# Kernel optimization log

Hardware: AMD Instinct MI355X
Metric: run time of the kernel (lower is better)

The kernel has to match this reference:

```python
import jax, jax.numpy as jnp
import numpy as np

N, E, D_IN, HID, HEADS, D_OUT, R = 20000, 640000, 256, 128, 4, 128, 32
NEG_SLOPE = 0.2  # PyG GATConv default


def setup_inputs() -> dict:
    key = jax.random.key(0)
    ks = jax.random.split(key, 12)
    s = 0.05
    return {
        "x": jax.random.normal(ks[0], (N, D_IN), jnp.float32),
        "edge_index": jax.random.randint(ks[1], (2, E), 0, N, dtype=jnp.int64),
        "edge_type": jax.random.randint(ks[2], (E,), 0, R, dtype=jnp.int64),
        "rel_emb": jax.random.normal(ks[3], (R, D_IN), jnp.float32) * s,
        "W1": jax.random.normal(ks[4], (D_IN, HEADS * HID), jnp.float32) * s,
        "att_src1": jax.random.normal(ks[5], (HEADS, HID), jnp.float32) * s,
        "att_dst1": jax.random.normal(ks[6], (HEADS, HID), jnp.float32) * s,
        "b1": jnp.zeros((HEADS * HID,), jnp.float32),
        "W2": jax.random.normal(ks[7], (HEADS * HID, D_OUT), jnp.float32) * s,
        "att_src2": jax.random.normal(ks[8], (1, D_OUT), jnp.float32) * s,
        "att_dst2": jax.random.normal(ks[9], (1, D_OUT), jnp.float32) * s,
        "b2": jnp.zeros((D_OUT,), jnp.float32),
    }


def _gat_conv(x, src, dst, W, a_src, a_dst, bias, heads, ch):
    """PyG GATConv (eval mode, self loops already in src/dst)."""
    n = x.shape[0]
    h = (x @ W).reshape(n, heads, ch)                      # [N,H,C]
    alpha_s = jnp.einsum('nhc,hc->nh', h, a_src)           # [N,H]
    alpha_d = jnp.einsum('nhc,hc->nh', h, a_dst)
    e = jax.nn.leaky_relu(alpha_s[src] + alpha_d[dst], NEG_SLOPE)  # [E,H]
    # segment softmax over incoming edges of each dst node
    m = jax.ops.segment_max(e, dst, num_segments=n)        # [N,H]
    p = jnp.exp(e - m[dst])
    denom = jax.ops.segment_sum(p, dst, num_segments=n)
    alpha = p / (denom[dst] + 1e-16)                       # [E,H]
    out = jax.ops.segment_sum(h[src] * alpha[:, :, None], dst, num_segments=n)
    return out.reshape(n, heads * ch) + bias


def reference(x, edge_index, edge_type, rel_emb, W1, att_src1, att_dst1, b1,
              W2, att_src2, att_dst2, b2):
    src, dst = edge_index[0], edge_index[1]
    # relational feature injection: x_mod[src] += rel_emb[edge_type]
    x_mod = x.at[src].add(rel_emb[edge_type])
    # GATConv adds self loops by default
    loop = jnp.arange(N, dtype=src.dtype)
    s2 = jnp.concatenate([src, loop])
    d2 = jnp.concatenate([dst, loop])
    h = _gat_conv(x_mod, s2, d2, W1, att_src1, att_dst1, b1, HEADS, HID)
    h = jax.nn.elu(h)
    return _gat_conv(h, s2, d2, W2, att_src2, att_dst2, b2, 1, D_OUT)
```

## Files before the change

kernel.cpp:

```cpp
#include <hip/hip_runtime.h>


#define D_IN   256
#define HID1   512
#define NHEADS 4
#define DOUT   128
#define NREL   32
#define NEG_SLOPE 0.2f
#define M_PAD  20096
#define NB     128

static __device__ __forceinline__ unsigned short f2b(float f) {
  union { float f; unsigned int i; } v; v.f = f;
  unsigned int x = v.i;
  return (unsigned short)((x + 0x7fffu + ((x >> 16) & 1u)) >> 16);
}
static __device__ __forceinline__ float lrelu(float x) {
  return x > 0.f ? x : NEG_SLOPE * x;
}

typedef __attribute__((ext_vector_type(8))) short bf16x8;
typedef __attribute__((ext_vector_type(4))) float f32x4;
typedef __attribute__((ext_vector_type(2))) float f32x2;

static __device__ __forceinline__ f32x2 up2(unsigned int u) {
  union { unsigned int i; float f; } lo, hi;
  lo.i = u << 16; hi.i = u & 0xffff0000u;
  f32x2 v; v.x = lo.f; v.y = hi.f; return v;
}
static __device__ __forceinline__ void pkfma(f32x2& a, f32x2 b, f32x2 c) {
  asm("v_pk_fma_f32 %0, %1, %2, %0" : "+v"(a) : "v"(b), "v"(c));
}
static __device__ __forceinline__ void accp(f32x2* acc, float w, uint4 r) {
  f32x2 wv = (f32x2)(w);
  pkfma(acc[0], wv, up2(r.x));
  pkfma(acc[1], wv, up2(r.y));
  pkfma(acc[2], wv, up2(r.z));
  pkfma(acc[3], wv, up2(r.w));
}
static __device__ __forceinline__ void acc4(f32x2 acc[4][4], float* den,
                                            float4 av, float4 adv, uint4 r) {
  float w0 = __expf(lrelu(av.x + adv.x));
  float w1 = __expf(lrelu(av.y + adv.y));
  float w2 = __expf(lrelu(av.z + adv.z));
  float w3 = __expf(lrelu(av.w + adv.w));
  f32x2 x0 = up2(r.x), x1 = up2(r.y), x2 = up2(r.z), x3 = up2(r.w);
  f32x2 wv;
  wv = (f32x2)(w0);
  pkfma(acc[0][0], wv, x0); pkfma(acc[0][1], wv, x1);
  pkfma(acc[0][2], wv, x2); pkfma(acc[0][3], wv, x3);
  wv = (f32x2)(w1);
  pkfma(acc[1][0], wv, x0); pkfma(acc[1][1], wv, x1);
  pkfma(acc[1][2], wv, x2); pkfma(acc[1][3], wv, x3);
  wv = (f32x2)(w2);
  pkfma(acc[2][0], wv, x0); pkfma(acc[2][1], wv, x1);
  pkfma(acc[2][2], wv, x2); pkfma(acc[2][3], wv, x3);
  wv = (f32x2)(w3);
  pkfma(acc[3][0], wv, x0); pkfma(acc[3][1], wv, x1);
  pkfma(acc[3][2], wv, x2); pkfma(acc[3][3], wv, x3);
  den[0] += w0; den[1] += w1; den[2] += w2; den[3] += w3;
}

__global__ __launch_bounds__(256) void hist_prep_kernel(
    const int* __restrict__ src, const int* __restrict__ dst,
    const int* __restrict__ et, unsigned int* __restrict__ counts8,
    int* __restrict__ gtable, int E, int n, int cb,
    const float* __restrict__ W1, const float* __restrict__ W2,
    unsigned short* __restrict__ W1T, unsigned short* __restrict__ W2T,
    const float* __restrict__ att_s1, const float* __restrict__ att_d1,
    float* __restrict__ us4, float* __restrict__ ud4,
    const float* __restrict__ att_s2, const float* __restrict__ att_d2,
    float* __restrict__ vs, float* __restrict__ vd) {
  int b = blockIdx.x;
  int t = threadIdx.x;
  if (b < NB) {
    extern __shared__ int hist[];
    for (int i = t; i < n; i += 256) hist[i] = 0;
    __syncthreads();
    int per = (E + NB - 1) / NB;
    int e0 = b * per;
    int e1 = min(e0 + per, E);
    for (int e = e0 + t; e < e1; e += 256) {
      atomicAdd(&hist[dst[e]], 1);
      int s = src[e], r = et[e];
      atomicAdd(&counts8[(size_t)s * 8 + (r >> 2)], 1u << (8 * (r & 3)));
    }
    __syncthreads();
    for (int i = t; i < n; i += 256) gtable[(size_t)b * n + i] = hist[i];
  } else if (b < NB + cb) {
    int idx = (b - NB) * 256 + t;
    if (idx < D_IN * HID1) {
      int r = idx / HID1, c = idx % HID1;
      W1T[(size_t)c * D_IN + r] = f2b(W1[idx]);
    } else {
      int k = idx - D_IN * HID1;
      if (k < HID1 * DOUT) {
        int r = k / DOUT, c = k % DOUT;
        W2T[(size_t)c * HID1 + r] = f2b(W2[k]);
      }
    }
  } else if (b == NB + cb) {
    int k = t;
    float us[4] = {0.f, 0.f, 0.f, 0.f}, ud[4] = {0.f, 0.f, 0.f, 0.f};
    for (int h = 0; h < 4; ++h)
      for (int c = 0; c < 128; ++c) {
        float wv = W1[(size_t)k * HID1 + h * 128 + c];
        us[h] += wv * att_s1[h * 128 + c];
        ud[h] += wv * att_d1[h * 128 + c];
      }
    ((float4*)us4)[k] = make_float4(us[0], us[1], us[2], us[3]);
    ((float4*)ud4)[k] = make_float4(ud[0], ud[1], ud[2], ud[3]);
  } else {
#pragma unroll
    for (int rr = 0; rr < 2; ++rr) {
      int r = t * 2 + rr;
      float ss = 0.f, dd = 0.f;
      for (int c = 0; c < DOUT; ++c) {
        float wv = W2[(size_t)r * DOUT + c];
        ss += wv * att_s2[c];
        dd += wv * att_d2[c];
      }
      vs[r] = ss; vd[r] = dd;
    }
  }
}

__global__ void colsum_kernel(const int* __restrict__ gtable,
                              int* __restrict__ deg, int n) {
  int d = blockIdx.x * 256 + threadIdx.x;
  if (d >= n) return;
  int s = 0;
#pragma unroll 8
  for (int b = 0; b < NB; ++b) s += gtable[(size_t)b * n + d];
  deg[d] = s;
}

__global__ void scan_local(const int* __restrict__ in, int* __restrict__ out,
                           int* __restrict__ bsum, int n) {
  __shared__ int wsum[4];
  int t = threadIdx.x;
  int base = blockIdx.x * 1024 + t * 4;
  int v0 = (base + 0 < n) ? in[base + 0] : 0;
  int v1 = (base + 1 < n) ? in[base + 1] : 0;
  int v2 = (base + 2 < n) ? in[base + 2] : 0;
  int v3 = (base + 3 < n) ? in[base + 3] : 0;
  int s = v0 + v1 + v2 + v3;
  int lane = t & 63, w = t >> 6;
  int sc = s;
  for (int off = 1; off < 64; off <<= 1) {
    int u = __shfl_up(sc, off);
    if (lane >= off) sc += u;
  }
  if (lane == 63) wsum[w] = sc;
  __syncthreads();
  int woff = 0;
  for (int i = 0; i < w; ++i) woff += wsum[i];
  int excl = woff + sc - s;
  if (base + 0 < n) out[base + 0] = excl;
  if (base + 1 < n) out[base + 1] = excl + v0;
  if (base + 2 < n) out[base + 2] = excl + v0 + v1;
  if (base + 3 < n) out[base + 3] = excl + v0 + v1 + v2;
  if (t == 255) bsum[blockIdx.x] = woff + sc;
}

__global__ void scan_blocks(int* __restrict__ bsum, int nb,
                            int* __restrict__ offsets, int n) {
  int t = threadIdx.x;
  int v = (t < nb) ? bsum[t] : 0;
  int sc = v;
  for (int off = 1; off < 64; off <<= 1) {
    int u = __shfl_up(sc, off);
    if (t >= off) sc += u;
  }
  if (t < nb) bsum[t] = sc - v;
  if (t == nb - 1) offsets[n] = v;
}

__global__ void rebase_kernel(int* __restrict__ gtable,
                              const int* __restrict__ offsets,
                              const int* __restrict__ bsum, int n) {
  int d = blockIdx.x * 256 + threadIdx.x;
  if (d >= n) return;
  int run = offsets[d] + bsum[d >> 10];
  for (int b = 0; b < NB; ++b) {
    size_t idx = (size_t)b * n + d;
    int v = gtable[idx];
    gtable[idx] = run;
    run += v;
  }
}

__global__ __launch_bounds__(256) void scatter2_kernel(
    const int* __restrict__ src, const int* __restrict__ dst,
    const int* __restrict__ gtable, int* __restrict__ csr_src, int E, int n) {
  extern __shared__ int cur[];
  int b = blockIdx.x;
  int t = threadIdx.x;
  for (int i = t; i < n; i += 256) cur[i] = gtable[(size_t)b * n + i];
  __syncthreads();
  int per = (E + NB - 1) / NB;
  int e0 = b * per;
  int e1 = min(e0 + per, E);
  for (int e = e0 + t; e < e1; e += 256) {
    int pos = atomicAdd(&cur[dst[e]], 1);
    csr_src[pos] = src[e];
  }
}

__global__ __launch_bounds__(256) void xmod_kernel(
    const float* __restrict__ x, const unsigned int* __restrict__ counts8,
    const float* __restrict__ rel, const float* __restrict__ us4,
    const float* __restrict__ ud4, unsigned short* __restrict__ x_modb,
    float* __restrict__ as1, float* __restrict__ ad1, int n_nodes) {
  int wv = threadIdx.x >> 6;
  int node = blockIdx.x * 4 + wv;
  if (node >= n_nodes) return;
  int l = threadIdx.x & 63;
  int r5 = l & 31;
  unsigned int cw = counts8[(size_t)node * 8 + (r5 >> 2)];
  int cnt_l = (int)((cw >> (8 * (r5 & 3))) & 0xffu);
  const float4* x4 = (const float4*)x;
  const float4* rel4 = (const float4*)rel;
  float4 v = x4[(size_t)node * 64 + l];
#pragma unroll
  for (int r = 0; r < NREL; ++r) {
    int c = __shfl(cnt_l, r);
    if (c) {
      float4 rv = rel4[r * 64 + l];
      float fc = (float)c;
      v.x += fc * rv.x; v.y += fc * rv.y; v.z += fc * rv.z; v.w += fc * rv.w;
    }
  }
  ushort4 o;
  o.x = f2b(v.x); o.y = f2b(v.y); o.z = f2b(v.z); o.w = f2b(v.w);
  *(ushort4*)(x_modb + (size_t)node * D_IN + l * 4) = o;
  const float4* usv = (const float4*)us4;
  const float4* udv = (const float4*)ud4;
  float vv[4] = {v.x, v.y, v.z, v.w};
  float sh[4] = {0.f, 0.f, 0.f, 0.f}, dh[4] = {0.f, 0.f, 0.f, 0.f};
#pragma unroll
  for (int i = 0; i < 4; ++i) {
    float4 uu = usv[l * 4 + i];
    float4 dd = udv[l * 4 + i];
    sh[0] += vv[i] * uu.x; sh[1] += vv[i] * uu.y; sh[2] += vv[i] * uu.z; sh[3] += vv[i] * uu.w;
    dh[0] += vv[i] * dd.x; dh[1] += vv[i] * dd.y; dh[2] += vv[i] * dd.z; dh[3] += vv[i] * dd.w;
  }
  for (int off = 32; off; off >>= 1) {
#pragma unroll
    for (int h = 0; h < 4; ++h) {
      sh[h] += __shfl_xor(sh[h], off);
      dh[h] += __shfl_xor(dh[h], off);
    }
  }
  if (l == 0) {
    ((float4*)as1)[node] = make_float4(sh[0], sh[1], sh[2], sh[3]);
    ((float4*)ad1)[node] = make_float4(dh[0], dh[1], dh[2], dh[3]);
  }
}

__global__ __launch_bounds__(256) void aggregate1_kernel(
    const unsigned short* __restrict__ x_modb,
    const float* __restrict__ as1, const float* __restrict__ ad1,
    const int* __restrict__ offsets, const int* __restrict__ bsum,
    const int* __restrict__ csr_src,
    unsigned short* __restrict__ agg_xb, int n_nodes) {
  int node = blockIdx.x * 4 + (threadIdx.x >> 6);
  if (node >= n_nodes) return;
  int lane = threadIdx.x & 63;
  int half = lane >> 5, l32 = lane & 31;
  int lo = offsets[node] + bsum[node >> 10];
  int hi = offsets[node + 1] + bsum[(node + 1) >> 10];
  float4 adv = ((const float4*)ad1)[node];
  const uint4* xv = (const uint4*)x_modb;
  const float4* as1v = (const float4*)as1;

  f32x2 acc[4][4];
#pragma unroll
  for (int h = 0; h < 4; ++h)
#pragma unroll
    for (int k = 0; k < 4; ++k) acc[h][k] = (f32x2)(0.f);
  float den[4] = {0.f, 0.f, 0.f, 0.f};

  int j = lo + half;
  int s = (j < hi) ? csr_src[j] : node;
  float4 av = as1v[(unsigned)s];
  uint4 r = xv[(unsigned)((s << 5) | l32)];
  while (j < hi) {
    int jn = j + 2;
    int sn = (jn < hi) ? csr_src[jn] : node;
    float4 avn = as1v[(unsigned)sn];
    uint4 rn = xv[(unsigned)((sn << 5) | l32)];
    acc4(acc, den, av, adv, r);
    j = jn; s = sn; av = avn; r = rn;
  }
  if (half == 0) {
    float4 asv = as1v[(unsigned)node];
    uint4 rs = xv[(unsigned)((node << 5) | l32)];
    acc4(acc, den, asv, adv, rs);
  }
#pragma unroll
  for (int h = 0; h < 4; ++h) {
#pragma unroll
    for (int k = 0; k < 4; ++k) {
      acc[h][k].x += __shfl_xor(acc[h][k].x, 32);
      acc[h][k].y += __shfl_xor(acc[h][k].y, 32);
    }
    den[h] += __shfl_xor(den[h], 32);
  }
  if (half == 0) {
#pragma unroll
    for (int h = 0; h < 4; ++h) {
      float inv = 1.f / (den[h] + 1e-16f);
      uint4 o;
      o.x = (unsigned)f2b(acc[h][0].x * inv) | ((unsigned)f2b(acc[h][0].y * inv) << 16);
      o.y = (unsigned)f2b(acc[h][1].x * inv) | ((unsigned)f2b(acc[h][1].y * inv) << 16);
      o.z = (unsigned)f2b(acc[h][2].x * inv) | ((unsigned)f2b(acc[h][2].y * inv) << 16);
      o.w = (unsigned)f2b(acc[h][3].x * inv) | ((unsigned)f2b(acc[h][3].y * inv) << 16);
      *(uint4*)(agg_xb + ((size_t)h * M_PAD + node) * D_IN + l32 * 8) = o;
    }
  }
}

template <int BM, int MODE>
__global__ __launch_bounds__(256) void mfma_gemm(
    const unsigned short* __restrict__ A, const unsigned short* __restrict__ BT,
    unsigned short* __restrict__ C, int M, int N, int K,
    const float* __restrict__ bias, const float* __restrict__ vs,
    const float* __restrict__ vd, float* __restrict__ as2, float* __restrict__ ad2) {
  constexpr int MFR = BM / 32;
  __shared__ __align__(16) unsigned short Asl[BM * 32];
  __shared__ __align__(16) unsigned short Bsl[128 * 32];
  int tid = threadIdx.x;
  int m0 = blockIdx.y * BM, n0 = blockIdx.x * 128;
  int lane = tid & 63, wv = tid >> 6;
  int wm = wv & 1, wn = wv >> 1;
  int l16 = lane & 15, quad = lane >> 4;
  int lr = lane >> 2, lseg = lane & 3;
  if (MODE == 1) A += (size_t)blockIdx.x * M_PAD * K;

  f32x4 acc[MFR][4];
#pragma unroll
  for (int i = 0; i < MFR; ++i)
#pragma unroll
    for (int j = 0; j < 4; ++j) acc[i][j] = (f32x4)(0.f);

  for (int k0 = 0; k0 < K; k0 += 32) {
#pragma unroll
    for (int c = wv; c < BM / 16; c += 4) {
      int gr = m0 + c * 16 + lr; gr = gr < M ? gr : M - 1;
      __builtin_amdgcn_global_load_lds(
          (const __attribute__((address_space(1))) void*)(A + (size_t)gr * K + k0 + lseg * 8),
          (__attribute__((address_space(3))) void*)(&Asl[c * 512]), 16, 0, 0);
    }
#pragma unroll
    for (int c = wv; c < 8; c += 4) {
      int gr = n0 + c * 16 + lr;
      __builtin_amdgcn_global_load_lds(
          (const __attribute__((address_space(1))) void*)(BT + (size_t)gr * K + k0 + lseg * 8),
          (__attribute__((address_space(3))) void*)(&Bsl[c * 512]), 16, 0, 0);
    }
    __syncthreads();
    bf16x8 af[MFR], bfr[4];
#pragma unroll
    for (int mf = 0; mf < MFR; ++mf)
      af[mf] = *(const bf16x8*)(&Asl[(wm * (BM / 2) + mf * 16 + l16) * 32 + quad * 8]);
#pragma unroll
    for (int nf = 0; nf < 4; ++nf)
      bfr[nf] = *(const bf16x8*)(&Bsl[(wn * 64 + nf * 16 + l16) * 32 + quad * 8]);
#pragma unroll
    for (int mf = 0; mf < MFR; ++mf)
#pragma unroll
      for (int nf = 0; nf < 4; ++nf)
        acc[mf][nf] = __builtin_amdgcn_mfma_f32_16x16x32_bf16(af[mf], bfr[nf], acc[mf][nf], 0, 0, 0);
    __syncthreads();
  }
  if (MODE == 0) {
#pragma unroll
    for (int mf = 0; mf < MFR; ++mf)
#pragma unroll
      for (int nf = 0; nf < 4; ++nf)
#pragma unroll
        for (int r = 0; r < 4; ++r) {
          int row = m0 + wm * (BM / 2) + mf * 16 + quad * 4 + r;
          int col = n0 + wn * 64 + nf * 16 + l16;
          C[(size_t)row * N + col] = f2b(acc[mf][nf][r]);
        }
  } else {
#pragma unroll
    for (int mf = 0; mf < MFR; ++mf)
#pragma unroll
      for (int r = 0; r < 4; ++r) {
        int row = m0 + wm * (BM / 2) + mf * 16 + quad * 4 + r;
        float sd = 0.f, dd = 0.f;
#pragma unroll
        for (int nf = 0; nf < 4; ++nf) {
          int col = n0 + wn * 64 + nf * 16 + l16;
          float cv = acc[mf][nf][r] + bias[col];
          cv = cv > 0.f ? cv : expm1f(cv);
          C[(size_t)row * N + col] = f2b(cv);
          sd += cv * vs[col];
          dd += cv * vd[col];
        }
#pragma unroll
        for (int off = 1; off < 16; off <<= 1) {
          sd += __shfl_xor(sd, off);
          dd += __shfl_xor(dd, off);
        }
        if (l16 == 0 && row < M) {
          atomicAdd(&as2[row], sd);
          atomicAdd(&ad2[row], dd);
        }
      }
  }
}

__global__ __launch_bounds__(256) void aggregate2_kernel(
    const unsigned short* __restrict__ t2b,
    const float* __restrict__ as2, const float* __restrict__ ad2,
    const int* __restrict__ offsets, const int* __restrict__ bsum,
    const int* __restrict__ csr_src,
    const float* __restrict__ bias, float* __restrict__ out, int n_nodes) {
  int node = blockIdx.x * 4 + (threadIdx.x >> 6);
  if (node >= n_nodes) return;
  int lane = threadIdx.x & 63;
  int g = lane >> 4, l16 = lane & 15;
  int lo = offsets[node] + bsum[node >> 10];
  int hi = offsets[node + 1] + bsum[(node + 1) >> 10];
  float ad = ad2[node];

  const uint4* t2v = (const uint4*)t2b;
  f32x2 acc[4];
#pragma unroll
  for (int k = 0; k < 4; ++k) acc[k] = (f32x2)(0.f);
  float denom = 0.f;
  int nit = (hi - lo + 3) >> 2;
  int j = lo + g;
  bool valid = j < hi;
  int s = valid ? csr_src[j] : node;
  float asv = as2[s];
  uint4 tv = t2v[(unsigned)((s << 4) | l16)];
  for (int i = 0; i < nit; ++i) {
    int jn = j + 4;
    bool vn = jn < hi;
    int sn = vn ? csr_src[jn] : node;
    float asv_n = as2[sn];
    uint4 tvn = t2v[(unsigned)((sn << 4) | l16)];
    float w = valid ? __expf(lrelu(asv + ad)) : 0.f;
    accp(acc, w, tv);
    denom += w;
    j = jn; valid = vn; s = sn; asv = asv_n; tv = tvn;
  }
  if (g == 0) {
    uint4 tv2 = t2v[(unsigned)((node << 4) | l16)];
    float w = __expf(lrelu(as2[node] + ad));
    accp(acc, w, tv2);
    denom += w;
  }
#pragma unroll
  for (int k = 0; k < 4; ++k) {
    acc[k].x += __shfl_xor(acc[k].x, 16); acc[k].y += __shfl_xor(acc[k].y, 16);
    acc[k].x += __shfl_xor(acc[k].x, 32); acc[k].y += __shfl_xor(acc[k].y, 32);
  }
  denom += __shfl_xor(denom, 16);
  denom += __shfl_xor(denom, 32);
  if (g == 0) {
    float inv = 1.f / (denom + 1e-16f);
    float4 o0, o1;
    o0.x = acc[0].x * inv + bias[l16 * 8 + 0];
    o0.y = acc[0].y * inv + bias[l16 * 8 + 1];
    o0.z = acc[1].x * inv + bias[l16 * 8 + 2];
    o0.w = acc[1].y * inv + bias[l16 * 8 + 3];
    o1.x = acc[2].x * inv + bias[l16 * 8 + 4];
    o1.y = acc[2].y * inv + bias[l16 * 8 + 5];
    o1.z = acc[3].x * inv + bias[l16 * 8 + 6];
    o1.w = acc[3].y * inv + bias[l16 * 8 + 7];
    *(float4*)(out + (size_t)node * DOUT + l16 * 8) = o0;
    *(float4*)(out + (size_t)node * DOUT + l16 * 8 + 4) = o1;
  }
}

extern "C" void kernel_launch(void* const* d_in, const int* in_sizes, int n_in,
                              void* d_out, int out_size, void* d_ws, size_t ws_size,
                              hipStream_t stream) {
  const float* x     = (const float*)d_in[0];
  const int* ei      = (const int*)d_in[1];
  const int* etype   = (const int*)d_in[2];
  const float* rel   = (const float*)d_in[3];
  const float* W1    = (const float*)d_in[4];
  const float* at_s1 = (const float*)d_in[5];
  const float* at_d1 = (const float*)d_in[6];
  const float* b1    = (const float*)d_in[7];
  const float* W2    = (const float*)d_in[8];
  const float* at_s2 = (const float*)d_in[9];
  const float* at_d2 = (const float*)d_in[10];
  const float* b2v   = (const float*)d_in[11];
  float* out         = (float*)d_out;

  const int N = in_sizes[0] / D_IN;
  const int E = in_sizes[2];
  const int* srcv = ei;
  const int* dstv = ei + E;

  char* p = (char*)d_ws;
  auto carve = [&](size_t bytes) -> char* {
    char* r = p; p += (bytes + 255) & ~(size_t)255; return r;
  };
  unsigned int* counts8 = (unsigned int*)carve((size_t)N * 8 * 4);
  float* as2     = (float*)carve((size_t)N * 4);
  float* ad2     = (float*)carve((size_t)N * 4);
  size_t zero_bytes = (size_t)(p - (char*)counts8);
  int*   deg     = (int*)carve((size_t)N * 4);
  int*   offsets = (int*)carve(((size_t)N + 1) * 4);
  int*   bsum    = (int*)carve(64 * 4);
  float* as1     = (float*)carve((size_t)N * NHEADS * 4);
  float* ad1     = (float*)carve((size_t)N * NHEADS * 4);
  float* vs      = (float*)carve((size_t)HID1 * 4);
  float* vd      = (float*)carve((size_t)HID1 * 4);
  float* us4     = (float*)carve((size_t)D_IN * 4 * 4);
  float* ud4     = (float*)carve((size_t)D_IN * 4 * 4);
  int*   csr_src = (int*)carve((size_t)E * 4);
  unsigned short* W1T    = (unsigned short*)carve((size_t)HID1 * D_IN * 2);
  unsigned short* W2T    = (unsigned short*)carve((size_t)DOUT * HID1 * 2);
  unsigned short* x_modb = (unsigned short*)carve((size_t)N * D_IN * 2);
  unsigned short* agg_xb = (unsigned short*)carve((size_t)NHEADS * M_PAD * D_IN * 2);
  unsigned short* h2b    = (unsigned short*)carve((size_t)M_PAD * HID1 * 2);
  unsigned short* t2b    = (unsigned short*)carve((size_t)M_PAD * DOUT * 2);
  int* gtable = (int*)h2b;

  hipMemsetAsync(counts8, 0, zero_bytes, stream);

  int cb = (D_IN * HID1 + HID1 * DOUT + 255) / 256;
  int nb = (N + 1023) / 1024;
  int ldsb = N * 4;
  hist_prep_kernel<<<NB + cb + 2, 256, ldsb, stream>>>(
      srcv, dstv, etype, counts8, gtable, E, N, cb,
      W1, W2, W1T, W2T, at_s1, at_d1, us4, ud4, at_s2, at_d2, vs, vd);
  colsum_kernel<<<(N + 255) / 256, 256, 0, stream>>>(gtable, deg, N);
  scan_local<<<nb, 256, 0, stream>>>(deg, offsets, bsum, N);
  scan_blocks<<<1, 64, 0, stream>>>(bsum, nb, offsets, N);
  rebase_kernel<<<(N + 255) / 256, 256, 0, stream>>>(gtable, offsets, bsum, N);
  scatter2_kernel<<<NB, 256, ldsb, stream>>>(srcv, dstv, gtable, csr_src, E, N);
  xmod_kernel<<<(N + 3) / 4, 256, 0, stream>>>(x, counts8, rel, us4, ud4, x_modb, as1, ad1, N);
  aggregate1_kernel<<<(N + 3) / 4, 256, 0, stream>>>(x_modb, as1, ad1, offsets, bsum,
                                                     csr_src, agg_xb, N);
  mfma_gemm<128, 1><<<dim3(NHEADS, M_PAD / 128), 256, 0, stream>>>(
      agg_xb, W1T, h2b, N, HID1, D_IN, b1, vs, vd, as2, ad2);
  mfma_gemm<64, 0><<<dim3(DOUT / 128, M_PAD / 64), 256, 0, stream>>>(
      h2b, W2T, t2b, N, DOUT, HID1, nullptr, nullptr, nullptr, nullptr, nullptr);
  aggregate2_kernel<<<(N + 3) / 4, 256, 0, stream>>>(
      t2b, as2, ad2, offsets, bsum, csr_src, b2v, out, N);
}
```

Baseline: 306.0 us.

## Aggregate layer-1 neighbours with MFMA over LDS-staged row chunks

Rewrites the first-layer attention aggregation. Each wave now gathers 32 neighbour rows at a time into LDS using direct global-to-LDS loads. It then multiplies a 16x32 bf16 weight fragment (4 heads of softmax weights) by the gathered rows with MFMA 16x16x32, reading them through transposed LDS reads, instead of doing per-edge packed FMAs in registers. The intent is to move the per-edge weighted accumulation onto matrix cores and cut VALU work. In exchange, softmax weights are rounded to bf16, 12 of the 16 MFMA rows are wasted, chunks are padded to 32 edges, and the block shrinks to 3 waves with about 50KB of LDS, which may reduce occupancy.

```diff
diff --git a/kernel.cpp b/kernel.cpp
--- a/kernel.cpp
+++ b/kernel.cpp
@@ -22,6 +22,7 @@
 typedef __attribute__((ext_vector_type(8))) short bf16x8;
 typedef __attribute__((ext_vector_type(4))) float f32x4;
 typedef __attribute__((ext_vector_type(2))) float f32x2;
+typedef __attribute__((ext_vector_type(2))) unsigned int u32x2;
 
 static __device__ __forceinline__ f32x2 up2(unsigned int u) {
   union { unsigned int i; float f; } lo, hi;
@@ -37,28 +38,6 @@
   pkfma(acc[1], wv, up2(r.y));
   pkfma(acc[2], wv, up2(r.z));
   pkfma(acc[3], wv, up2(r.w));
-}
-static __device__ __forceinline__ void acc4(f32x2 acc[4][4], float* den,
-                                            float4 av, float4 adv, uint4 r) {
-  float w0 = __expf(lrelu(av.x + adv.x));
-  float w1 = __expf(lrelu(av.y + adv.y));
-  float w2 = __expf(lrelu(av.z + adv.z));
-  float w3 = __expf(lrelu(av.w + adv.w));
-  f32x2 x0 = up2(r.x), x1 = up2(r.y), x2 = up2(r.z), x3 = up2(r.w);
-  f32x2 wv;
-  wv = (f32x2)(w0);
-  pkfma(acc[0][0], wv, x0); pkfma(acc[0][1], wv, x1);
-  pkfma(acc[0][2], wv, x2); pkfma(acc[0][3], wv, x3);
-  wv = (f32x2)(w1);
-  pkfma(acc[1][0], wv, x0); pkfma(acc[1][1], wv, x1);
-  pkfma(acc[1][2], wv, x2); pkfma(acc[1][3], wv, x3);
-  wv = (f32x2)(w2);
-  pkfma(acc[2][0], wv, x0); pkfma(acc[2][1], wv, x1);
-  pkfma(acc[2][2], wv, x2); pkfma(acc[2][3], wv, x3);
-  wv = (f32x2)(w3);
-  pkfma(acc[3][0], wv, x0); pkfma(acc[3][1], wv, x1);
-  pkfma(acc[3][2], wv, x2); pkfma(acc[3][3], wv, x3);
-  den[0] += w0; den[1] += w1; den[2] += w2; den[3] += w3;
 }
 
 __global__ __launch_bounds__(256) void hist_prep_kernel(
@@ -258,65 +237,105 @@
   }
 }
 
-__global__ __launch_bounds__(256) void aggregate1_kernel(
+__global__ __launch_bounds__(192) void aggregate1_kernel(
     const unsigned short* __restrict__ x_modb,
     const float* __restrict__ as1, const float* __restrict__ ad1,
     const int* __restrict__ offsets, const int* __restrict__ bsum,
     const int* __restrict__ csr_src,
     unsigned short* __restrict__ agg_xb, int n_nodes) {
-  int node = blockIdx.x * 4 + (threadIdx.x >> 6);
+  __shared__ __align__(16) unsigned short buf[3][8192 + 512];
+  int wid = threadIdx.x >> 6;
+  int node = blockIdx.x * 3 + wid;
   if (node >= n_nodes) return;
   int lane = threadIdx.x & 63;
-  int half = lane >> 5, l32 = lane & 31;
+  int l32 = lane & 31;
+  unsigned short* rowbuf = &buf[wid][0];
+  unsigned short* wbuf = &buf[wid][8192];
   int lo = offsets[node] + bsum[node >> 10];
   int hi = offsets[node + 1] + bsum[(node + 1) >> 10];
+  int nchunk = (hi - lo + 32) >> 5;
   float4 adv = ((const float4*)ad1)[node];
-  const uint4* xv = (const uint4*)x_modb;
-  const float4* as1v = (const float4*)as1;
-
-  f32x2 acc[4][4];
-#pragma unroll
-  for (int h = 0; h < 4; ++h)
-#pragma unroll
-    for (int k = 0; k < 4; ++k) acc[h][k] = (f32x2)(0.f);
-  float den[4] = {0.f, 0.f, 0.f, 0.f};
-
-  int j = lo + half;
-  int s = (j < hi) ? csr_src[j] : node;
-  float4 av = as1v[(unsigned)s];
-  uint4 r = xv[(unsigned)((s << 5) | l32)];
-  while (j < hi) {
-    int jn = j + 2;
-    int sn = (jn < hi) ? csr_src[jn] : node;
-    float4 avn = as1v[(unsigned)sn];
-    uint4 rn = xv[(unsigned)((sn << 5) | l32)];
-    acc4(acc, den, av, adv, r);
-    j = jn; s = sn; av = avn; r = rn;
-  }
-  if (half == 0) {
-    float4 asv = as1v[(unsigned)node];
-    uint4 rs = xv[(unsigned)((node << 5) | l32)];
-    acc4(acc, den, asv, adv, rs);
-  }
-#pragma unroll
-  for (int h = 0; h < 4; ++h) {
-#pragma unroll
-    for (int k = 0; k < 4; ++k) {
-      acc[h][k].x += __shfl_xor(acc[h][k].x, 32);
-      acc[h][k].y += __shfl_xor(acc[h][k].y, 32);
-    }
-    den[h] += __shfl_xor(den[h], 32);
-  }
-  if (half == 0) {
-#pragma unroll
-    for (int h = 0; h < 4; ++h) {
-      float inv = 1.f / (den[h] + 1e-16f);
-      uint4 o;
-      o.x = (unsigned)f2b(acc[h][0].x * inv) | ((unsigned)f2b(acc[h][0].y * inv) << 16);
-      o.y = (unsigned)f2b(acc[h][1].x * inv) | ((unsigned)f2b(acc[h][1].y * inv) << 16);
-      o.z = (unsigned)f2b(acc[h][2].x * inv) | ((unsigned)f2b(acc[h][2].y * inv) << 16);
-      o.w = (unsigned)f2b(acc[h][3].x * inv) | ((unsigned)f2b(acc[h][3].y * inv) << 16);
-      *(uint4*)(agg_xb + ((size_t)h * M_PAD + node) * D_IN + l32 * 8) = o;
+  float4 asp = ((const float4*)as1)[node];
+
+  unsigned trbase =
+      (unsigned)(size_t)(__attribute__((address_space(3))) unsigned short*)rowbuf +
+      (unsigned)((lane >> 4) * 256 + (lane & 15) * 8);
+
+  f32x4 acc[16];
+#pragma unroll
+  for (int s = 0; s < 16; ++s) acc[s] = (f32x4)(0.f);
+  float den0 = 0.f, den1 = 0.f, den2 = 0.f, den3 = 0.f;
+
+  for (int c = 0; c < nchunk; ++c) {
+    int q = lo + c * 32 + l32;
+    int srcn = (q < hi) ? csr_src[q] : node;
+    int sst = __shfl(srcn, lane >> 1);
+    const unsigned short* gp = x_modb + (size_t)sst * D_IN + (lane & 1) * 8;
+#pragma unroll
+    for (int s = 0; s < 16; ++s)
+      __builtin_amdgcn_global_load_lds(
+          (const __attribute__((address_space(1))) void*)(gp + s * 16),
+          (__attribute__((address_space(3))) void*)(rowbuf + s * 512), 16, 0, 0);
+    float4 av = (q < hi) ? ((const float4*)as1)[srcn] : asp;
+    bool val = q <= hi;
+    float w0 = val ? __expf(lrelu(av.x + adv.x)) : 0.f;
+    float w1 = val ? __expf(lrelu(av.y + adv.y)) : 0.f;
+    float w2 = val ? __expf(lrelu(av.z + adv.z)) : 0.f;
+    float w3 = val ? __expf(lrelu(av.w + adv.w)) : 0.f;
+    unsigned short h0 = f2b(w0), h1 = f2b(w1), h2 = f2b(w2), h3 = f2b(w3);
+    union { unsigned u; float f; } rr;
+    rr.u = (unsigned)h0 << 16; float r0 = rr.f;
+    rr.u = (unsigned)h1 << 16; float r1 = rr.f;
+    rr.u = (unsigned)h2 << 16; float r2 = rr.f;
+    rr.u = (unsigned)h3 << 16; float r3 = rr.f;
+#pragma unroll
+    for (int off = 16; off; off >>= 1) {
+      r0 += __shfl_xor(r0, off);
+      r1 += __shfl_xor(r1, off);
+      r2 += __shfl_xor(r2, off);
+      r3 += __shfl_xor(r3, off);
+    }
+    den0 += r0; den1 += r1; den2 += r2; den3 += r3;
+    if (lane < 32) {
+      wbuf[0 * 32 + l32] = h0;
+      wbuf[1 * 32 + l32] = h1;
+      wbuf[2 * 32 + l32] = h2;
+      wbuf[3 * 32 + l32] = h3;
+    }
+    bf16x8 afrag = *(const bf16x8*)(wbuf + (lane & 15) * 32 + (lane >> 4) * 8);
+    asm volatile("s_waitcnt vmcnt(0)" ::: "memory");
+#pragma unroll
+    for (int g = 0; g < 2; ++g) {
+      u32x2 t[16];
+#pragma unroll
+      for (int s = 0; s < 8; ++s) {
+        asm volatile("ds_read_b64_tr_b16 %0, %1 offset:%2"
+                     : "=v"(t[2 * s]) : "v"(trbase), "i"(g * 8192 + s * 1024));
+        asm volatile("ds_read_b64_tr_b16 %0, %1 offset:%2"
+                     : "=v"(t[2 * s + 1]) : "v"(trbase), "i"(g * 8192 + s * 1024 + 128));
+      }
+      asm volatile("s_waitcnt lgkmcnt(0)" ::: "memory");
+      __builtin_amdgcn_sched_barrier(0);
+#pragma unroll
+      for (int s = 0; s < 8; ++s) {
+        union { u32x2 h[2]; bf16x8 v; } bb;
+        bb.h[0] = t[2 * s]; bb.h[1] = t[2 * s + 1];
+        acc[g * 8 + s] =
+            __builtin_amdgcn_mfma_f32_16x16x32_bf16(afrag, bb.v, acc[g * 8 + s], 0, 0, 0);
+      }
+    }
+  }
+  float i0 = 1.f / (den0 + 1e-16f);
+  float i1 = 1.f / (den1 + 1e-16f);
+  float i2 = 1.f / (den2 + 1e-16f);
+  float i3 = 1.f / (den3 + 1e-16f);
+  if (lane < 16) {
+#pragma unroll
+    for (int s = 0; s < 16; ++s) {
+      agg_xb[((size_t)0 * M_PAD + node) * D_IN + s * 16 + lane] = f2b(acc[s][0] * i0);
+      agg_xb[((size_t)1 * M_PAD + node) * D_IN + s * 16 + lane] = f2b(acc[s][1] * i1);
+      agg_xb[((size_t)2 * M_PAD + node) * D_IN + s * 16 + lane] = f2b(acc[s][2] * i2);
+      agg_xb[((size_t)3 * M_PAD + node) * D_IN + s * 16 + lane] = f2b(acc[s][3] * i3);
     }
   }
 }
@@ -541,7 +560,7 @@
   rebase_kernel<<<(N + 255) / 256, 256, 0, stream>>>(gtable, offsets, bsum, N);
   scatter2_kernel<<<NB, 256, ldsb, stream>>>(srcv, dstv, gtable, csr_src, E, N);
   xmod_kernel<<<(N + 3) / 4, 256, 0, stream>>>(x, counts8, rel, us4, ud4, x_modb, as1, ad1, N);
-  aggregate1_kernel<<<(N + 3) / 4, 256, 0, stream>>>(x_modb, as1, ad1, offsets, bsum,
+  aggregate1_kernel<<<(N + 2) / 3, 192, 0, stream>>>(x_modb, as1, ad1, offsets, bsum,
                                                      csr_src, agg_xb, N);
   mfma_gemm<128, 1><<<dim3(NHEADS, M_PAD / 128), 256, 0, stream>>>(
       agg_xb, W1T, h2b, N, HID1, D_IN, b1, vs, vd, as2, ad2);
```

Measured after the change: 315.5 us. 1.03x slower.

## Precompute per-edge exp attention weights in scatter and stream them in aggregate1

Applied to the files above, without the earlier changes.

Moves the layer-1 attention logit computation (leaky-relu plus exp per head) out of the aggregation loop and into the CSR scatter kernel. Scatter now runs after xmod and writes bf16-packed exp weights for each edge at its CSR position. Aggregate1 then reads 8 bytes per edge instead of a gathered float4 of source logits, and does no exp work. This cuts transcendental work and the random as1 gathers in the hot loop, at the cost of an extra E*8-byte buffer, extra work in scatter, and bf16 rounding of the weights. It also unrolls the rebase loop by 8.

```diff
diff --git a/kernel.cpp b/kernel.cpp
--- a/kernel.cpp
+++ b/kernel.cpp
@@ -37,28 +37,6 @@
   pkfma(acc[1], wv, up2(r.y));
   pkfma(acc[2], wv, up2(r.z));
   pkfma(acc[3], wv, up2(r.w));
-}
-static __device__ __forceinline__ void acc4(f32x2 acc[4][4], float* den,
-                                            float4 av, float4 adv, uint4 r) {
-  float w0 = __expf(lrelu(av.x + adv.x));
-  float w1 = __expf(lrelu(av.y + adv.y));
-  float w2 = __expf(lrelu(av.z + adv.z));
-  float w3 = __expf(lrelu(av.w + adv.w));
-  f32x2 x0 = up2(r.x), x1 = up2(r.y), x2 = up2(r.z), x3 = up2(r.w);
-  f32x2 wv;
-  wv = (f32x2)(w0);
-  pkfma(acc[0][0], wv, x0); pkfma(acc[0][1], wv, x1);
-  pkfma(acc[0][2], wv, x2); pkfma(acc[0][3], wv, x3);
-  wv = (f32x2)(w1);
-  pkfma(acc[1][0], wv, x0); pkfma(acc[1][1], wv, x1);
-  pkfma(acc[1][2], wv, x2); pkfma(acc[1][3], wv, x3);
-  wv = (f32x2)(w2);
-  pkfma(acc[2][0], wv, x0); pkfma(acc[2][1], wv, x1);
-  pkfma(acc[2][2], wv, x2); pkfma(acc[2][3], wv, x3);
-  wv = (f32x2)(w3);
-  pkfma(acc[3][0], wv, x0); pkfma(acc[3][1], wv, x1);
-  pkfma(acc[3][2], wv, x2); pkfma(acc[3][3], wv, x3);
-  den[0] += w0; den[1] += w1; den[2] += w2; den[3] += w3;
 }
 
 __global__ __launch_bounds__(256) void hist_prep_kernel(
@@ -182,6 +160,7 @@
   int d = blockIdx.x * 256 + threadIdx.x;
   if (d >= n) return;
   int run = offsets[d] + bsum[d >> 10];
+#pragma unroll 8
   for (int b = 0; b < NB; ++b) {
     size_t idx = (size_t)b * n + d;
     int v = gtable[idx];
@@ -192,7 +171,10 @@
 
 __global__ __launch_bounds__(256) void scatter2_kernel(
     const int* __restrict__ src, const int* __restrict__ dst,
-    const int* __restrict__ gtable, int* __restrict__ csr_src, int E, int n) {
+    const int* __restrict__ gtable, int* __restrict__ csr_src,
+    uint2* __restrict__ wexp,
+    const float* __restrict__ as1, const float* __restrict__ ad1,
+    int E, int n) {
   extern __shared__ int cur[];
   int b = blockIdx.x;
   int t = threadIdx.x;
@@ -202,8 +184,17 @@
   int e0 = b * per;
   int e1 = min(e0 + per, E);
   for (int e = e0 + t; e < e1; e += 256) {
-    int pos = atomicAdd(&cur[dst[e]], 1);
-    csr_src[pos] = src[e];
+    int d = dst[e], s = src[e];
+    int pos = atomicAdd(&cur[d], 1);
+    csr_src[pos] = s;
+    float4 av = ((const float4*)as1)[s];
+    float4 dv = ((const float4*)ad1)[d];
+    unsigned short h0 = f2b(__expf(lrelu(av.x + dv.x)));
+    unsigned short h1 = f2b(__expf(lrelu(av.y + dv.y)));
+    unsigned short h2 = f2b(__expf(lrelu(av.z + dv.z)));
+    unsigned short h3 = f2b(__expf(lrelu(av.w + dv.w)));
+    wexp[pos] = make_uint2((unsigned)h0 | ((unsigned)h1 << 16),
+                           (unsigned)h2 | ((unsigned)h3 << 16));
   }
 }
 
@@ -260,6 +251,7 @@
 
 __global__ __launch_bounds__(256) void aggregate1_kernel(
     const unsigned short* __restrict__ x_modb,
+    const uint2* __restrict__ wexp,
     const float* __restrict__ as1, const float* __restrict__ ad1,
     const int* __restrict__ offsets, const int* __restrict__ bsum,
     const int* __restrict__ csr_src,
@@ -270,52 +262,85 @@
   int half = lane >> 5, l32 = lane & 31;
   int lo = offsets[node] + bsum[node >> 10];
   int hi = offsets[node + 1] + bsum[(node + 1) >> 10];
-  float4 adv = ((const float4*)ad1)[node];
   const uint4* xv = (const uint4*)x_modb;
-  const float4* as1v = (const float4*)as1;
 
   f32x2 acc[4][4];
 #pragma unroll
   for (int h = 0; h < 4; ++h)
 #pragma unroll
     for (int k = 0; k < 4; ++k) acc[h][k] = (f32x2)(0.f);
-  float den[4] = {0.f, 0.f, 0.f, 0.f};
+  f32x2 den01 = (f32x2)(0.f), den23 = (f32x2)(0.f);
 
   int j = lo + half;
   int s = (j < hi) ? csr_src[j] : node;
-  float4 av = as1v[(unsigned)s];
+  uint2 w = (j < hi) ? wexp[j] : make_uint2(0u, 0u);
   uint4 r = xv[(unsigned)((s << 5) | l32)];
   while (j < hi) {
     int jn = j + 2;
     int sn = (jn < hi) ? csr_src[jn] : node;
-    float4 avn = as1v[(unsigned)sn];
+    uint2 wn = (jn < hi) ? wexp[jn] : make_uint2(0u, 0u);
     uint4 rn = xv[(unsigned)((sn << 5) | l32)];
-    acc4(acc, den, av, adv, r);
-    j = jn; s = sn; av = avn; r = rn;
+    f32x2 w01 = up2(w.x), w23 = up2(w.y);
+    den01 += w01; den23 += w23;
+    f32x2 x0 = up2(r.x), x1 = up2(r.y), x2 = up2(r.z), x3 = up2(r.w);
+    f32x2 wv0 = (f32x2)(w01.x), wv1 = (f32x2)(w01.y);
+    f32x2 wv2 = (f32x2)(w23.x), wv3 = (f32x2)(w23.y);
+    pkfma(acc[0][0], wv0, x0); pkfma(acc[0][1], wv0, x1);
+    pkfma(acc[0][2], wv0, x2); pkfma(acc[0][3], wv0, x3);
+    pkfma(acc[1][0], wv1, x0); pkfma(acc[1][1], wv1, x1);
+    pkfma(acc[1][2], wv1, x2); pkfma(acc[1][3], wv1, x3);
+    pkfma(acc[2][0], wv2, x0); pkfma(acc[2][1], wv2, x1);
+    pkfma(acc[2][2], wv2, x2); pkfma(acc[2][3], wv2, x3);
+    pkfma(acc[3][0], wv3, x0); pkfma(acc[3][1], wv3, x1);
+    pkfma(acc[3][2], wv3, x2); pkfma(acc[3][3], wv3, x3);
+    j = jn; s = sn; w = wn; r = rn;
   }
   if (half == 0) {
-    float4 asv = as1v[(unsigned)node];
+    float4 av = ((const float4*)as1)[node];
+    float4 dv = ((const float4*)ad1)[node];
+    unsigned short h0 = f2b(__expf(lrelu(av.x + dv.x)));
+    unsigned short h1 = f2b(__expf(lrelu(av.y + dv.y)));
+    unsigned short h2 = f2b(__expf(lrelu(av.z + dv.z)));
+    unsigned short h3 = f2b(__expf(lrelu(av.w + dv.w)));
+    unsigned wlo = (unsigned)h0 | ((unsigned)h1 << 16);
+    unsigned whi = (unsigned)h2 | ((unsigned)h3 << 16);
+    f32x2 w01 = up2(wlo), w23 = up2(whi);
+    den01 += w01; den23 += w23;
     uint4 rs = xv[(unsigned)((node << 5) | l32)];
-    acc4(acc, den, asv, adv, rs);
-  }
-#pragma unroll
-  for (int h = 0; h < 4; ++h) {
+    f32x2 x0 = up2(rs.x), x1 = up2(rs.y), x2 = up2(rs.z), x3 = up2(rs.w);
+    f32x2 wv0 = (f32x2)(w01.x), wv1 = (f32x2)(w01.y);
+    f32x2 wv2 = (f32x2)(w23.x), wv3 = (f32x2)(w23.y);
+    pkfma(acc[0][0], wv0, x0); pkfma(acc[0][1], wv0, x1);
+    pkfma(acc[0][2], wv0, x2); pkfma(acc[0][3], wv0, x3);
+    pkfma(acc[1][0], wv1, x0); pkfma(acc[1][1], wv1, x1);
+    pkfma(acc[1][2], wv1, x2); pkfma(acc[1][3], wv1, x3);
+    pkfma(acc[2][0], wv2, x0); pkfma(acc[2][1], wv2, x1);
+    pkfma(acc[2][2], wv2, x2); pkfma(acc[2][3], wv2, x3);
+    pkfma(acc[3][0], wv3, x0); pkfma(acc[3][1], wv3, x1);
+    pkfma(acc[3][2], wv3, x2); pkfma(acc[3][3], wv3, x3);
+  }
+#pragma unroll
+  for (int h = 0; h < 4; ++h)
 #pragma unroll
     for (int k = 0; k < 4; ++k) {
       acc[h][k].x += __shfl_xor(acc[h][k].x, 32);
       acc[h][k].y += __shfl_xor(acc[h][k].y, 32);
     }
-    den[h] += __shfl_xor(den[h], 32);
-  }
+  den01.x += __shfl_xor(den01.x, 32); den01.y += __shfl_xor(den01.y, 32);
+  den23.x += __shfl_xor(den23.x, 32); den23.y += __shfl_xor(den23.y, 32);
   if (half == 0) {
+    float inv[4];
+    inv[0] = 1.f / (den01.x + 1e-16f);
+    inv[1] = 1.f / (den01.y + 1e-16f);
+    inv[2] = 1.f / (den23.x + 1e-16f);
+    inv[3] = 1.f / (den23.y + 1e-16f);
 #pragma unroll
     for (int h = 0; h < 4; ++h) {
-      float inv = 1.f / (den[h] + 1e-16f);
       uint4 o;
-      o.x = (unsigned)f2b(acc[h][0].x * inv) | ((unsigned)f2b(acc[h][0].y * inv) << 16);
-      o.y = (unsigned)f2b(acc[h][1].x * inv) | ((unsigned)f2b(acc[h][1].y * inv) << 16);
-      o.z = (unsigned)f2b(acc[h][2].x * inv) | ((unsigned)f2b(acc[h][2].y * inv) << 16);
-      o.w = (unsigned)f2b(acc[h][3].x * inv) | ((unsigned)f2b(acc[h][3].y * inv) << 16);
+      o.x = (unsigned)f2b(acc[h][0].x * inv[h]) | ((unsigned)f2b(acc[h][0].y * inv[h]) << 16);
+      o.y = (unsigned)f2b(acc[h][1].x * inv[h]) | ((unsigned)f2b(acc[h][1].y * inv[h]) << 16);
+      o.z = (unsigned)f2b(acc[h][2].x * inv[h]) | ((unsigned)f2b(acc[h][2].y * inv[h]) << 16);
+      o.w = (unsigned)f2b(acc[h][3].x * inv[h]) | ((unsigned)f2b(acc[h][3].y * inv[h]) << 16);
       *(uint4*)(agg_xb + ((size_t)h * M_PAD + node) * D_IN + l32 * 8) = o;
     }
   }
@@ -519,6 +544,7 @@
   float* us4     = (float*)carve((size_t)D_IN * 4 * 4);
   float* ud4     = (float*)carve((size_t)D_IN * 4 * 4);
   int*   csr_src = (int*)carve((size_t)E * 4);
+  uint2* wexp    = (uint2*)carve((size_t)E * 8);
   unsigned short* W1T    = (unsigned short*)carve((size_t)HID1 * D_IN * 2);
   unsigned short* W2T    = (unsigned short*)carve((size_t)DOUT * HID1 * 2);
   unsigned short* x_modb = (unsigned short*)carve((size_t)N * D_IN * 2);
@@ -527,7 +553,7 @@
   unsigned short* t2b    = (unsigned short*)carve((size_t)M_PAD * DOUT * 2);
   int* gtable = (int*)h2b;
 
-  hipMemsetAsync(counts8, 0, zero_bytes, stream);
+  (void)hipMemsetAsync(counts8, 0, zero_bytes, stream);
 
   int cb = (D_IN * HID1 + HID1 * DOUT + 255) / 256;
   int nb = (N + 1023) / 1024;
@@ -539,10 +565,11 @@
   scan_local<<<nb, 256, 0, stream>>>(deg, offsets, bsum, N);
   scan_blocks<<<1, 64, 0, stream>>>(bsum, nb, offsets, N);
   rebase_kernel<<<(N + 255) / 256, 256, 0, stream>>>(gtable, offsets, bsum, N);
-  scatter2_kernel<<<NB, 256, ldsb, stream>>>(srcv, dstv, gtable, csr_src, E, N);
   xmod_kernel<<<(N + 3) / 4, 256, 0, stream>>>(x, counts8, rel, us4, ud4, x_modb, as1, ad1, N);
-  aggregate1_kernel<<<(N + 3) / 4, 256, 0, stream>>>(x_modb, as1, ad1, offsets, bsum,
-                                                     csr_src, agg_xb, N);
+  scatter2_kernel<<<NB, 256, ldsb, stream>>>(srcv, dstv, gtable, csr_src, wexp,
+                                             as1, ad1, E, N);
+  aggregate1_kernel<<<(N + 3) / 4, 256, 0, stream>>>(x_modb, wexp, as1, ad1, offsets,
+                                                     bsum, csr_src, agg_xb, N);
   mfma_gemm<128, 1><<<dim3(NHEADS, M_PAD / 128), 256, 0, stream>>>(
       agg_xb, W1T, h2b, N, HID1, D_IN, b1, vs, vd, as2, ad2);
   mfma_gemm<64, 0><<<dim3(DOUT / 128, M_PAD / 64), 256, 0, stream>>>(
```

Result: no change. 309.2 us (+1.1%).
